# Optimization experiments

Measured on AMD Instinct MI355X. Metric: run time of the kernel, lower is better.

## Reference

```python
import jax, jax.numpy as jnp
import numpy as np

DT = 0.01  # time_delta from init
SIGMA, RHO, BETA = 10.0, 28.0, 8.0 / 3.0  # Lorenz parameters for self.function


def setup_inputs() -> dict:
    key = jax.random.key(0)
    # traj: [T, len_var, B] ensemble of trajectory states over time
    traj = jax.random.normal(key, (2048, 3, 8192), dtype=jnp.float32)
    return {"traj": traj}


def _jacobian(state):
    # state: [V, B] -> discrete tangent map I + DT * J_lorenz(state), shape [B, V, V]
    x, y, z = state[0], state[1], state[2]
    zero = jnp.zeros_like(x)
    one = jnp.ones_like(x)
    J = jnp.stack([
        jnp.stack([-SIGMA * one, SIGMA * one, zero], axis=-1),
        jnp.stack([RHO - z, -one, -x], axis=-1),
        jnp.stack([y, x, -BETA * one], axis=-1),
    ], axis=-2)  # [B, V, V]
    return jnp.eye(3, dtype=state.dtype) + DT * J


def _gram_schmidt_rows(M):
    # Row-wise Gram-Schmidt + normalization, exactly as the torch gram_schmidt
    # (in-place slicing makes it modified GS against already-orthogonalized rows)
    # followed by normalization(). M: [B, V, V]. Returns (Q [B,V,V], lognorms [V,B]).
    V = M.shape[-2]
    rows, lognorms = [], []
    for k in range(V):
        r = M[..., k, :]
        for q in rows:  # q already unit-norm -> projection coeff is just q.r
            r = r - jnp.sum(q * r, axis=-1, keepdims=True) * q
        n = jnp.sqrt(jnp.sum(r * r, axis=-1, keepdims=True))
        rows.append(r / n)
        lognorms.append(jnp.log(n[..., 0]))
    return jnp.stack(rows, axis=-2), jnp.stack(lognorms, axis=0)


def reference(traj):
    T, V, B = traj.shape
    Q0 = jnp.broadcast_to(jnp.eye(V, dtype=traj.dtype), (B, V, V))

    def step(Q, state):
        M = jnp.einsum('bij,bjk->bik', _jacobian(state), Q)  # eye = Jaco @ eye
        Qn, ln = _gram_schmidt_rows(M)
        return Qn, ln

    _, lns = jax.lax.scan(step, Q0, traj)  # lns: [T, V, B]
    # Running-average recurrence L_{k+1} = (L_k*k*dt + log n_k)/((k+1)*dt)
    # telescopes exactly to sum_k log(n_k) / (T * dt).
    return jnp.sum(lns, axis=0) / (T * DT)  # [V, B] Lyapunov spectrum per trajectory
```

## Files before the change

kernel.cpp:

```cpp
#include <hip/hip_runtime.h>

#define T_STEPS 2048
#define B_CH    8192
#define DT_F    0.01f
#define NCHUNK  32
#define CHUNK   (T_STEPS / NCHUNK)
#define WARM    64
#define TILE    8

__device__ __forceinline__ float fast_rsqrt(float x) { return __builtin_amdgcn_rsqf(x); }
__device__ __forceinline__ float fast_log2(float x)  { return __builtin_amdgcn_logf(x); }

struct Q9 { float q00,q01,q02,q10,q11,q12,q20,q21,q22; };

__device__ __forceinline__ void gs_step(float x, float y, float z, Q9& Q,
                                        float& P0, float& P1, float& P2) {
  const float a00 = 0.9f;
  const float a01 = 0.1f;
  const float a11 = 0.99f;
  const float a22 = 1.0f - DT_F * (8.0f / 3.0f);
  float a10 = DT_F * (28.0f - z);
  float a12 = -DT_F * x;
  float a20 = DT_F * y;
  float a21 = DT_F * x;

  float m00 = a00*Q.q00 + a01*Q.q10;
  float m01 = a00*Q.q01 + a01*Q.q11;
  float m02 = a00*Q.q02 + a01*Q.q12;
  float m10 = a10*Q.q00 + a11*Q.q10 + a12*Q.q20;
  float m11 = a10*Q.q01 + a11*Q.q11 + a12*Q.q21;
  float m12 = a10*Q.q02 + a11*Q.q12 + a12*Q.q22;
  float m20 = a20*Q.q00 + a21*Q.q10 + a22*Q.q20;
  float m21 = a20*Q.q01 + a21*Q.q11 + a22*Q.q21;
  float m22 = a20*Q.q02 + a21*Q.q12 + a22*Q.q22;

  float n0 = m00*m00 + m01*m01 + m02*m02;
  float d1 = m00*m10 + m01*m11 + m02*m12;
  float d2 = m00*m20 + m01*m21 + m02*m22;

  float i0 = fast_rsqrt(n0);
  float inv0 = i0 * i0;
  P0 *= n0;
  Q.q00 = m00*i0; Q.q01 = m01*i0; Q.q02 = m02*i0;

  float c1 = d1 * inv0;
  float r10 = m10 - c1*m00, r11 = m11 - c1*m01, r12 = m12 - c1*m02;
  float c2 = d2 * inv0;
  float r20 = m20 - c2*m00, r21 = m21 - c2*m01, r22 = m22 - c2*m02;

  float n1 = r10*r10 + r11*r11 + r12*r12;
  float d3 = r10*r20 + r11*r21 + r12*r22;
  float i1 = fast_rsqrt(n1);
  float inv1 = i1 * i1;
  P1 *= n1;
  Q.q10 = r10*i1; Q.q11 = r11*i1; Q.q12 = r12*i1;

  float c3 = d3 * inv1;
  float s20 = r20 - c3*r10, s21 = r21 - c3*r11, s22 = r22 - c3*r12;
  float n2 = s20*s20 + s21*s21 + s22*s22;
  float i2 = fast_rsqrt(n2);
  P2 *= n2;
  Q.q20 = s20*i2; Q.q21 = s21*i2; Q.q22 = s22*i2;
}

__global__ __attribute__((amdgpu_waves_per_eu(4, 4)))
__launch_bounds__(256) void lyap_chunk_kernel(const float* __restrict__ traj,
                                              float* __restrict__ ws) {
  const int b = blockIdx.x * 256 + threadIdx.x;
  const int chunk = blockIdx.y;
  const int warm = (chunk == 0) ? 0 : WARM;
  const int warmPer = warm / (2 * TILE);
  const int nper = (CHUNK + warm) / (2 * TILE);
  const float* __restrict__ p =
      traj + (size_t)(chunk * CHUNK - warm) * (3 * B_CH) + b;

  float sA[TILE][3], sB[TILE][3];
#pragma unroll
  for (int i = 0; i < TILE; ++i) {
    sA[i][0] = p[(i*3 + 0) * B_CH];
    sA[i][1] = p[(i*3 + 1) * B_CH];
    sA[i][2] = p[(i*3 + 2) * B_CH];
  }

  Q9 Q = {1.f,0.f,0.f, 0.f,1.f,0.f, 0.f,0.f,1.f};
  float S0 = 0.f, S1 = 0.f, S2 = 0.f;
  float B0 = 0.f, B1 = 0.f, B2 = 0.f;
  float P0 = 1.f, P1 = 1.f, P2 = 1.f;

  for (int per = 0; per < nper; ++per) {
    if (per == warmPer) { B0 = S0; B1 = S1; B2 = S2; }
    {
      const float* pt = p + (size_t)(2*per + 1) * (TILE*3*B_CH);
#pragma unroll
      for (int i = 0; i < TILE; ++i) {
        sB[i][0] = pt[(i*3 + 0) * B_CH];
        sB[i][1] = pt[(i*3 + 1) * B_CH];
        sB[i][2] = pt[(i*3 + 2) * B_CH];
      }
    }
#pragma unroll
    for (int i = 0; i < TILE; ++i)
      gs_step(sA[i][0], sA[i][1], sA[i][2], Q, P0, P1, P2);

    if (per + 1 < nper) {
      const float* pt = p + (size_t)(2*per + 2) * (TILE*3*B_CH);
#pragma unroll
      for (int i = 0; i < TILE; ++i) {
        sA[i][0] = pt[(i*3 + 0) * B_CH];
        sA[i][1] = pt[(i*3 + 1) * B_CH];
        sA[i][2] = pt[(i*3 + 2) * B_CH];
      }
    }
#pragma unroll
    for (int i = 0; i < TILE; ++i)
      gs_step(sB[i][0], sB[i][1], sB[i][2], Q, P0, P1, P2);

    S0 += fast_log2(P0); P0 = 1.f;
    S1 += fast_log2(P1); P1 = 1.f;
    S2 += fast_log2(P2); P2 = 1.f;
  }

  ws[(chunk*3 + 0) * B_CH + b] = S0 - B0;
  ws[(chunk*3 + 1) * B_CH + b] = S1 - B1;
  ws[(chunk*3 + 2) * B_CH + b] = S2 - B2;
}

__global__ __launch_bounds__(256) void lyap_reduce_kernel(const float* __restrict__ ws,
                                                          float* __restrict__ out) {
  const int i = blockIdx.x * 256 + threadIdx.x;
  float s = 0.f;
#pragma unroll
  for (int c = 0; c < NCHUNK; ++c) s += ws[c * 3 * B_CH + i];
  const float scale = 0.5f * 0.69314718055994531f / (T_STEPS * DT_F);
  out[i] = s * scale;
}

extern "C" void kernel_launch(void* const* d_in, const int* in_sizes, int n_in,
                              void* d_out, int out_size, void* d_ws, size_t ws_size,
                              hipStream_t stream) {
  (void)in_sizes; (void)n_in; (void)out_size; (void)ws_size;
  const float* traj = (const float*)d_in[0];
  float* out = (float*)d_out;
  float* ws  = (float*)d_ws;

  lyap_chunk_kernel<<<dim3(B_CH / 256, NCHUNK), dim3(256), 0, stream>>>(traj, ws);
  lyap_reduce_kernel<<<dim3(3 * B_CH / 256), dim3(256), 0, stream>>>(ws, out);
}
```

Baseline: 312.4 us.

## Process two trajectories per thread with packed float2 math and finer time chunks

Each thread now handles two adjacent trajectories using float2 vector types, so the multiply-adds can map to packed FP32 instructions and the loads become 8-byte wide. To keep the grid filled, the time axis is split into 64 chunks instead of 32, with the warm-up shortened to 32 steps and the tile size halved. The fixed waves-per-EU attribute is dropped. The shorter warm-up may change how closely the chunked result matches the reference, and the extra chunks add redundant warm-up work.

```diff
diff --git a/kernel.cpp b/kernel.cpp
--- a/kernel.cpp
+++ b/kernel.cpp
@@ -3,99 +3,107 @@
 #define T_STEPS 2048
 #define B_CH    8192
 #define DT_F    0.01f
-#define NCHUNK  32
+#define NCHUNK  64
 #define CHUNK   (T_STEPS / NCHUNK)
-#define WARM    64
-#define TILE    8
+#define WARM    32
+#define TILE    4
+
+typedef float v2f __attribute__((ext_vector_type(2)));
 
 __device__ __forceinline__ float fast_rsqrt(float x) { return __builtin_amdgcn_rsqf(x); }
 __device__ __forceinline__ float fast_log2(float x)  { return __builtin_amdgcn_logf(x); }
+__device__ __forceinline__ v2f v2_rsq(v2f n) {
+  v2f r; r.x = fast_rsqrt(n.x); r.y = fast_rsqrt(n.y); return r;
+}
 
-struct Q9 { float q00,q01,q02,q10,q11,q12,q20,q21,q22; };
+struct Q9 { v2f q00,q01,q02,q10,q11,q12,q20,q21,q22; };
 
-__device__ __forceinline__ void gs_step(float x, float y, float z, Q9& Q,
-                                        float& P0, float& P1, float& P2) {
+__device__ __forceinline__ void gs_step(v2f x, v2f y, v2f z, Q9& Q,
+                                        v2f& P0, v2f& P1, v2f& P2) {
   const float a00 = 0.9f;
   const float a01 = 0.1f;
   const float a11 = 0.99f;
   const float a22 = 1.0f - DT_F * (8.0f / 3.0f);
-  float a10 = DT_F * (28.0f - z);
-  float a12 = -DT_F * x;
-  float a20 = DT_F * y;
-  float a21 = DT_F * x;
+  v2f a10 = DT_F * (28.0f - z);
+  v2f a12 = -DT_F * x;
+  v2f a20 = DT_F * y;
+  v2f a21 = DT_F * x;
 
-  float m00 = a00*Q.q00 + a01*Q.q10;
-  float m01 = a00*Q.q01 + a01*Q.q11;
-  float m02 = a00*Q.q02 + a01*Q.q12;
-  float m10 = a10*Q.q00 + a11*Q.q10 + a12*Q.q20;
-  float m11 = a10*Q.q01 + a11*Q.q11 + a12*Q.q21;
-  float m12 = a10*Q.q02 + a11*Q.q12 + a12*Q.q22;
-  float m20 = a20*Q.q00 + a21*Q.q10 + a22*Q.q20;
-  float m21 = a20*Q.q01 + a21*Q.q11 + a22*Q.q21;
-  float m22 = a20*Q.q02 + a21*Q.q12 + a22*Q.q22;
+  v2f m00 = a00*Q.q00 + a01*Q.q10;
+  v2f m01 = a00*Q.q01 + a01*Q.q11;
+  v2f m02 = a00*Q.q02 + a01*Q.q12;
+  v2f m10 = a10*Q.q00 + a11*Q.q10 + a12*Q.q20;
+  v2f m11 = a10*Q.q01 + a11*Q.q11 + a12*Q.q21;
+  v2f m12 = a10*Q.q02 + a11*Q.q12 + a12*Q.q22;
+  v2f m20 = a20*Q.q00 + a21*Q.q10 + a22*Q.q20;
+  v2f m21 = a20*Q.q01 + a21*Q.q11 + a22*Q.q21;
+  v2f m22 = a20*Q.q02 + a21*Q.q12 + a22*Q.q22;
 
-  float n0 = m00*m00 + m01*m01 + m02*m02;
-  float d1 = m00*m10 + m01*m11 + m02*m12;
-  float d2 = m00*m20 + m01*m21 + m02*m22;
+  v2f n0 = m00*m00 + m01*m01 + m02*m02;
+  v2f d1 = m00*m10 + m01*m11 + m02*m12;
+  v2f d2 = m00*m20 + m01*m21 + m02*m22;
 
-  float i0 = fast_rsqrt(n0);
-  float inv0 = i0 * i0;
+  v2f i0 = v2_rsq(n0);
+  v2f inv0 = i0 * i0;
   P0 *= n0;
   Q.q00 = m00*i0; Q.q01 = m01*i0; Q.q02 = m02*i0;
 
-  float c1 = d1 * inv0;
-  float r10 = m10 - c1*m00, r11 = m11 - c1*m01, r12 = m12 - c1*m02;
-  float c2 = d2 * inv0;
-  float r20 = m20 - c2*m00, r21 = m21 - c2*m01, r22 = m22 - c2*m02;
+  v2f c1 = d1 * inv0;
+  v2f r10 = m10 - c1*m00, r11 = m11 - c1*m01, r12 = m12 - c1*m02;
+  v2f c2 = d2 * inv0;
+  v2f r20 = m20 - c2*m00, r21 = m21 - c2*m01, r22 = m22 - c2*m02;
 
-  float n1 = r10*r10 + r11*r11 + r12*r12;
-  float d3 = r10*r20 + r11*r21 + r12*r22;
-  float i1 = fast_rsqrt(n1);
-  float inv1 = i1 * i1;
+  v2f n1 = r10*r10 + r11*r11 + r12*r12;
+  v2f d3 = r10*r20 + r11*r21 + r12*r22;
+  v2f i1 = v2_rsq(n1);
+  v2f inv1 = i1 * i1;
   P1 *= n1;
   Q.q10 = r10*i1; Q.q11 = r11*i1; Q.q12 = r12*i1;
 
-  float c3 = d3 * inv1;
-  float s20 = r20 - c3*r10, s21 = r21 - c3*r11, s22 = r22 - c3*r12;
-  float n2 = s20*s20 + s21*s21 + s22*s22;
-  float i2 = fast_rsqrt(n2);
+  v2f c3 = d3 * inv1;
+  v2f s20 = r20 - c3*r10, s21 = r21 - c3*r11, s22 = r22 - c3*r12;
+  v2f n2 = s20*s20 + s21*s21 + s22*s22;
+  v2f i2 = v2_rsq(n2);
   P2 *= n2;
   Q.q20 = s20*i2; Q.q21 = s21*i2; Q.q22 = s22*i2;
 }
 
-__global__ __attribute__((amdgpu_waves_per_eu(4, 4)))
-__launch_bounds__(256) void lyap_chunk_kernel(const float* __restrict__ traj,
-                                              float* __restrict__ ws) {
-  const int b = blockIdx.x * 256 + threadIdx.x;
+__global__ __launch_bounds__(256) void lyap_chunk_kernel(const float* __restrict__ traj,
+                                                         float* __restrict__ ws) {
+  const int c = blockIdx.x * 256 + threadIdx.x;
   const int chunk = blockIdx.y;
   const int warm = (chunk == 0) ? 0 : WARM;
   const int warmPer = warm / (2 * TILE);
   const int nper = (CHUNK + warm) / (2 * TILE);
-  const float* __restrict__ p =
-      traj + (size_t)(chunk * CHUNK - warm) * (3 * B_CH) + b;
+  const int R = B_CH / 2;
+  const v2f* __restrict__ p =
+      (const v2f*)traj + (size_t)(chunk * CHUNK - warm) * (3 * R) + c;
 
-  float sA[TILE][3], sB[TILE][3];
+  v2f sA[TILE][3], sB[TILE][3];
 #pragma unroll
   for (int i = 0; i < TILE; ++i) {
-    sA[i][0] = p[(i*3 + 0) * B_CH];
-    sA[i][1] = p[(i*3 + 1) * B_CH];
-    sA[i][2] = p[(i*3 + 2) * B_CH];
+    sA[i][0] = p[(i*3 + 0) * R];
+    sA[i][1] = p[(i*3 + 1) * R];
+    sA[i][2] = p[(i*3 + 2) * R];
   }
 
-  Q9 Q = {1.f,0.f,0.f, 0.f,1.f,0.f, 0.f,0.f,1.f};
-  float S0 = 0.f, S1 = 0.f, S2 = 0.f;
-  float B0 = 0.f, B1 = 0.f, B2 = 0.f;
-  float P0 = 1.f, P1 = 1.f, P2 = 1.f;
+  Q9 Q;
+  Q.q00 = 1.f; Q.q01 = 0.f; Q.q02 = 0.f;
+  Q.q10 = 0.f; Q.q11 = 1.f; Q.q12 = 0.f;
+  Q.q20 = 0.f; Q.q21 = 0.f; Q.q22 = 1.f;
+  v2f S0 = 0.f, S1 = 0.f, S2 = 0.f;
+  v2f B0 = 0.f, B1 = 0.f, B2 = 0.f;
+  v2f P0 = 1.f, P1 = 1.f, P2 = 1.f;
 
   for (int per = 0; per < nper; ++per) {
     if (per == warmPer) { B0 = S0; B1 = S1; B2 = S2; }
     {
-      const float* pt = p + (size_t)(2*per + 1) * (TILE*3*B_CH);
+      const v2f* pt = p + (size_t)(2*per + 1) * (TILE * 3 * R);
 #pragma unroll
       for (int i = 0; i < TILE; ++i) {
-        sB[i][0] = pt[(i*3 + 0) * B_CH];
-        sB[i][1] = pt[(i*3 + 1) * B_CH];
-        sB[i][2] = pt[(i*3 + 2) * B_CH];
+        sB[i][0] = pt[(i*3 + 0) * R];
+        sB[i][1] = pt[(i*3 + 1) * R];
+        sB[i][2] = pt[(i*3 + 2) * R];
       }
     }
 #pragma unroll
@@ -103,26 +111,27 @@
       gs_step(sA[i][0], sA[i][1], sA[i][2], Q, P0, P1, P2);
 
     if (per + 1 < nper) {
-      const float* pt = p + (size_t)(2*per + 2) * (TILE*3*B_CH);
+      const v2f* pt = p + (size_t)(2*per + 2) * (TILE * 3 * R);
 #pragma unroll
       for (int i = 0; i < TILE; ++i) {
-        sA[i][0] = pt[(i*3 + 0) * B_CH];
-        sA[i][1] = pt[(i*3 + 1) * B_CH];
-        sA[i][2] = pt[(i*3 + 2) * B_CH];
+        sA[i][0] = pt[(i*3 + 0) * R];
+        sA[i][1] = pt[(i*3 + 1) * R];
+        sA[i][2] = pt[(i*3 + 2) * R];
       }
     }
 #pragma unroll
     for (int i = 0; i < TILE; ++i)
       gs_step(sB[i][0], sB[i][1], sB[i][2], Q, P0, P1, P2);
 
-    S0 += fast_log2(P0); P0 = 1.f;
-    S1 += fast_log2(P1); P1 = 1.f;
-    S2 += fast_log2(P2); P2 = 1.f;
+    S0.x += fast_log2(P0.x); S0.y += fast_log2(P0.y); P0 = 1.f;
+    S1.x += fast_log2(P1.x); S1.y += fast_log2(P1.y); P1 = 1.f;
+    S2.x += fast_log2(P2.x); S2.y += fast_log2(P2.y); P2 = 1.f;
   }
 
-  ws[(chunk*3 + 0) * B_CH + b] = S0 - B0;
-  ws[(chunk*3 + 1) * B_CH + b] = S1 - B1;
-  ws[(chunk*3 + 2) * B_CH + b] = S2 - B2;
+  v2f* __restrict__ wsv = (v2f*)ws;
+  wsv[(chunk*3 + 0) * R + c] = S0 - B0;
+  wsv[(chunk*3 + 1) * R + c] = S1 - B1;
+  wsv[(chunk*3 + 2) * R + c] = S2 - B2;
 }
 
 __global__ __launch_bounds__(256) void lyap_reduce_kernel(const float* __restrict__ ws,
@@ -143,6 +152,6 @@
   float* out = (float*)d_out;
   float* ws  = (float*)d_ws;
 
-  lyap_chunk_kernel<<<dim3(B_CH / 256, NCHUNK), dim3(256), 0, stream>>>(traj, ws);
+  lyap_chunk_kernel<<<dim3(B_CH / 512, NCHUNK), dim3(256), 0, stream>>>(traj, ws);
   lyap_reduce_kernel<<<dim3(3 * B_CH / 256), dim3(256), 0, stream>>>(ws, out);
 }
```

Result: faster. 295.9 us (-5.3%).
